# Performance work log

Measured on AMD Instinct MI355X. Metric: run time of the kernel, lower is better.

The kernel has to match this reference:

```python
import jax, jax.numpy as jnp
import numpy as np

EMBED_DIM = 64
NUM_GROUPS = 16
KEY_DIM = 64
WAVE_LENGTH = 1000.0


def setup_inputs() -> dict:
    key = jax.random.key(0)
    ks = jax.random.split(key, 8)
    N, R, D = 4, 512, 1024
    features = jax.random.normal(ks[0], (N, R, D), dtype=jnp.float32)
    # valid boxes: ymin/xmin in [0,800), heights/widths in [1,201)
    u = jax.random.uniform(ks[1], (N, R, 4), dtype=jnp.float32)
    ymin = u[..., 0] * 800.0
    xmin = u[..., 1] * 800.0
    ymax = ymin + 1.0 + u[..., 2] * 200.0
    xmax = xmin + 1.0 + u[..., 3] * 200.0
    boxes = jnp.stack([ymin, xmin, ymax, xmax], axis=-1)  # [N,R,4]
    s = 0.02
    geo_w = jax.random.normal(ks[2], (EMBED_DIM, NUM_GROUPS), dtype=jnp.float32) * s
    geo_b = jnp.zeros((NUM_GROUPS,), dtype=jnp.float32)
    Wq = jax.random.normal(ks[3], (D, KEY_DIM), dtype=jnp.float32) * s
    bq = jnp.zeros((KEY_DIM,), dtype=jnp.float32)
    Wk = jax.random.normal(ks[4], (D, KEY_DIM), dtype=jnp.float32) * s
    bk = jnp.zeros((KEY_DIM,), dtype=jnp.float32)
    Wv = jax.random.normal(ks[5], (D, D // NUM_GROUPS), dtype=jnp.float32) * s
    bv = jnp.zeros((D // NUM_GROUPS,), dtype=jnp.float32)
    return {"features": features, "boxes": boxes, "geo_w": geo_w, "geo_b": geo_b,
            "Wq": Wq, "bq": bq, "Wk": Wk, "bk": bk, "Wv": Wv, "bv": bv}


def _geometry_embeddings(boxes):
    # boxes: [N,R,4] -> embeddings [N,R,R,EMBED_DIM]
    ymin, xmin, ymax, xmax = jnp.split(boxes, 4, axis=2)  # each [N,R,1]
    height = ymax - ymin + 1.0
    width = xmax - xmin + 1.0
    cy = 0.5 * (ymin + ymax)
    cx = 0.5 * (xmin + xmax)
    cyT = jnp.transpose(cy, (0, 2, 1))
    cxT = jnp.transpose(cx, (0, 2, 1))
    dy = jnp.log(jnp.maximum((cy - cyT) / height, 1e-5))          # [N,R,R]
    dx = jnp.log(jnp.maximum((cx - cxT) / width, 1e-5))
    dh = jnp.log(height / jnp.transpose(height, (0, 2, 1)))
    dw = jnp.log(width / jnp.transpose(width, (0, 2, 1)))
    pos = jnp.stack([dy, dx, dh, dw], axis=3)                     # [N,R,R,4]
    feat_range = jnp.arange(EMBED_DIM // 8, dtype=jnp.float32)
    dim_mat = jnp.power(WAVE_LENGTH, (8.0 / EMBED_DIM) * feat_range)  # [8]
    div = (100.0 * pos)[..., None] / dim_mat                      # [N,R,R,4,8]
    emb = jnp.concatenate([jnp.sin(div), jnp.cos(div)], axis=4)   # [N,R,R,4,16]
    N, R = boxes.shape[0], boxes.shape[1]
    return emb.reshape(N, R, R, EMBED_DIM)


def reference(features, boxes, geo_w, geo_b, Wq, bq, Wk, bk, Wv, bv):
    N, R, D = features.shape
    G = NUM_GROUPS
    dk = KEY_DIM // G  # per-group key dim
    emb = _geometry_embeddings(boxes)                              # [N,R,R,E]
    # 1x1 conv + relu over pairwise embedding channels
    geometry_weight = jax.nn.relu(jnp.einsum('nqke,eg->nqkg', emb, geo_w) + geo_b)
    geometry_weight = jnp.transpose(geometry_weight, (0, 1, 3, 2))  # [N,R,G,R]
    q = (features @ Wq + bq).reshape(N, R, G, dk)
    k = (features @ Wk + bk).reshape(N, R, G, dk)
    v = features @ Wv + bv                                          # [N,R,D/G]
    dot = jnp.einsum('nqgd,nkgd->ngqk', q, k) / jnp.sqrt(jnp.float32(dk))
    appearance_weight = jnp.transpose(dot, (0, 2, 1, 3))            # [N,R,G,R]
    relation = jnp.log(jnp.maximum(geometry_weight, 1e-6)) + appearance_weight
    relation = jax.nn.softmax(relation, axis=3)                     # [N,R,G,R]
    out = jnp.einsum('nqgk,nkv->nqgv', relation, v)                 # [N,R,G,D/G]
    out = out.reshape(N, R, D)
    return features + out
```

## Files before the change

### kernel.cpp

```cpp
#include <hip/hip_runtime.h>
#include <stdint.h>

#define R_ 512
#define D_ 1024
#define G_ 16
#define NT 256

typedef __attribute__((ext_vector_type(8))) short short8;
typedef __attribute__((ext_vector_type(4))) float floatx4;

#if __has_builtin(__builtin_amdgcn_fractf)
#define FRACT(x) __builtin_amdgcn_fractf(x)
#else
#define FRACT(x) ((x) - floorf(x))
#endif

__device__ __forceinline__ unsigned pk2bf(float a, float b) {
    unsigned ua = __builtin_bit_cast(unsigned, a) + 0x8000u;
    unsigned ub = __builtin_bit_cast(unsigned, b) + 0x8000u;
    return (ub & 0xFFFF0000u) | (ua >> 16);
}
__device__ __forceinline__ unsigned short f2bf(float a) {
    return (unsigned short)((__builtin_bit_cast(unsigned, a) + 0x8000u) >> 16);
}

__global__ __launch_bounds__(256) void prep_kernel(
    const float* __restrict__ Wq, const float* __restrict__ Wk,
    const float* __restrict__ Wv, const float* __restrict__ geo_w,
    const float* __restrict__ boxes,
    unsigned short* __restrict__ WTb, unsigned short* __restrict__ geoF,
    float4* __restrict__ bp4, float2* __restrict__ bp2, int NR)
{
    const int b = blockIdx.x, t = threadIdx.x;
    if (b < 48) {
        __shared__ float s[64][65];
        const int mat = b >> 4, rblk = b & 15;
        const float* Wsrc = (mat == 0) ? Wq : (mat == 1) ? Wk : Wv;
        const int d0 = rblk * 64;
        #pragma unroll
        for (int i = 0; i < 16; i++) {
            int e = t + i * 256;
            s[e >> 6][e & 63] = Wsrc[(size_t)(d0 + (e >> 6)) * 64 + (e & 63)];
        }
        __syncthreads();
        #pragma unroll
        for (int i = 0; i < 16; i++) {
            int e = t + i * 256;
            int c = e >> 6, r = e & 63;
            WTb[(size_t)(mat * 64 + c) * 1024 + d0 + r] = f2bf(s[r][c]);
        }
    } else if (b == 48) {
        #pragma unroll
        for (int i = 0; i < 4; i++) {
            int idx = t * 4 + i;
            int h = idx >> 9, rem = idx & 511, ll = rem >> 3, j = rem & 7;
            int e = h * 32 + (ll >> 4) * 8 + j, cc = ll & 15;
            geoF[idx] = f2bf(geo_w[e * G_ + cc]);
        }
    } else {
        int r = (b - 49) * 256 + t;
        if (r < NR) {
            float ymin = boxes[r*4+0], xmin = boxes[r*4+1];
            float ymax = boxes[r*4+2], xmax = boxes[r*4+3];
            float h = ymax - ymin + 1.0f, w = xmax - xmin + 1.0f;
            bp4[r] = make_float4(0.5f * (ymin + ymax), 0.5f * (xmin + xmax),
                                 __logf(h), __logf(w));
            bp2[r] = make_float2(1.0f / h, 1.0f / w);
        }
    }
}

__global__ __launch_bounds__(256) void proj_kernel(
    const float* __restrict__ feat, const unsigned short* __restrict__ WTb,
    const float* __restrict__ bq, const float* __restrict__ bk,
    const float* __restrict__ bv,
    unsigned short* __restrict__ qd16, unsigned short* __restrict__ kb16,
    unsigned short* __restrict__ vT16)
{
    __shared__ __align__(16) unsigned short s_A[16][1032];

    const int t = threadIdx.x, l = t & 63, w = t >> 6;
    const int mb = blockIdx.x / 3, ng = blockIdx.x % 3;
    const long row0 = (long)mb * 16;

    const float4* f4 = (const float4*)(feat + row0 * D_);
    #pragma unroll
    for (int i = 0; i < 16; i++) {
        int e = t + i * 256;
        int row = e >> 8, c4 = e & 255;
        float4 v = f4[e];
        uint2 pk;
        pk.x = pk2bf(v.x, v.y);
        pk.y = pk2bf(v.z, v.w);
        *(uint2*)&s_A[row][c4 * 4] = pk;
    }
    __syncthreads();

    const int lc = l & 15, q = l >> 4;
    const int gcol = (ng * 4 + w) * 16 + lc;
    const unsigned short* bptr = WTb + (size_t)gcol * 1024 + q * 8;

    floatx4 acc = {0.f, 0.f, 0.f, 0.f};
    #pragma unroll 8
    for (int k0 = 0; k0 < 1024; k0 += 32) {
        short8 a  = *(const short8*)&s_A[lc][k0 + q * 8];
        short8 bb = *(const short8*)(bptr + k0);
        acc = __builtin_amdgcn_mfma_f32_16x16x32_bf16(a, bb, acc, 0, 0, 0);
    }

    const int mat = gcol >> 6, mcol = gcol & 63;
    const float* B = (mat == 0) ? bq : (mat == 1) ? bk : bv;
    const float bias = B[mcol];
    #pragma unroll
    for (int r = 0; r < 4; r++) {
        long gr = row0 + q * 4 + r;
        float val = acc[r] + bias;
        if (mat == 0)      qd16[gr * 64 + mcol] = f2bf(0.5f * val);
        else if (mat == 1) kb16[gr * 64 + mcol] = f2bf(val);
        else               vT16[((size_t)((gr >> 9) * 64 + mcol)) * 512 + (gr & 511)] = f2bf(val);
    }
}

__global__ __launch_bounds__(256, 4) void relation_kernel(
    const float* __restrict__ feat, const float* __restrict__ geo_b,
    const unsigned short* __restrict__ geoF, const unsigned short* __restrict__ qd16,
    const unsigned short* __restrict__ kb16, const unsigned short* __restrict__ vT16,
    const float4* __restrict__ bp4, const float2* __restrict__ bp2,
    float* __restrict__ out)
{
    __shared__ __align__(16) unsigned short s_p[2][16][520];
    __shared__ float s_reds[2][4][16];

    const int t = threadIdx.x;
    const int l = t & 63;
    const int w = t >> 6;
    const int c = l & 15;
    const int quad = l >> 4;
    const int nqA = blockIdx.x * 2, nqB = nqA + 1;
    const int n = nqA >> 9;

    const float4 qbA = bp4[nqA], qbB = bp4[nqB];
    const float2 qiA = bp2[nqA], qiB = bp2[nqB];
    const float gbias = geo_b[c];
    const floatx4 ginit = {gbias, gbias, gbias, gbias};

    short8 bgeo0 = *(const short8*)(geoF + l * 8);
    short8 bgeo1 = *(const short8*)(geoF + 512 + l * 8);

    const bool act = (quad == ((c >> 1) & 3));
    const int hsel = c >> 3, jhalf = c & 1;
    uint2 qvA = *(const uint2*)(qd16 + (size_t)nqA * 64 + c * 4);
    uint2 qvB = *(const uint2*)(qd16 + (size_t)nqB * 64 + c * 4);
    short qA[4] = {(short)(qvA.x & 0xFFFF), (short)(qvA.x >> 16),
                   (short)(qvA.y & 0xFFFF), (short)(qvA.y >> 16)};
    short qB[4] = {(short)(qvB.x & 0xFFFF), (short)(qvB.x >> 16),
                   (short)(qvB.y & 0xFFFF), (short)(qvB.y >> 16)};
    short8 bqfA0, bqfA1, bqfB0, bqfB1;
    #pragma unroll
    for (int j = 0; j < 8; j++) {
        bool on0 = act && (hsel == 0) && ((j >> 2) == jhalf);
        bool on1 = act && (hsel == 1) && ((j >> 2) == jhalf);
        bqfA0[j] = on0 ? qA[j & 3] : (short)0;
        bqfA1[j] = on1 ? qA[j & 3] : (short)0;
        bqfB0[j] = on0 ? qB[j & 3] : (short)0;
        bqfB1[j] = on1 ? qB[j & 3] : (short)0;
    }

    const float C8[8] = {
        15.91549431f,
        15.91549431f * 0.4216965034f,
        15.91549431f * 0.1778279410f,
        15.91549431f * 0.0749894209f,
        15.91549431f * 0.0316227766f,
        15.91549431f * 0.0133352143f,
        15.91549431f * 0.0056234133f,
        15.91549431f * 0.0023713737f };

    const float offs = (quad & 1) ? 0.25f : 0.0f;
    const bool qlow = (quad < 2);

    float sumA = 0.f, sumB = 0.f;
    const int krow0 = n * R_ + w * 128;

    #pragma unroll
    for (int ti = 0; ti < 8; ti++) {
        float4 kb = bp4[krow0 + ti * 16 + c];

        float aA  = qlow ? (qbA.x - kb.x) * qiA.x : (qbA.y - kb.y) * qiA.y;
        float pAa = __logf(fmaxf(aA, 1e-5f));
        float pAb = qlow ? (qbA.z - kb.z) : (qbA.w - kb.w);
        float aB  = qlow ? (qbB.x - kb.x) * qiB.x : (qbB.y - kb.y) * qiB.y;
        float pBa = __logf(fmaxf(aB, 1e-5f));
        float pBb = qlow ? (qbB.z - kb.z) : (qbB.w - kb.w);

        uint4 uA0, uA1, uB0, uB1;
        #pragma unroll
        for (int jj = 0; jj < 4; jj++) {
            float r0, r1;
            r0 = FRACT(fmaf(pAa, C8[2*jj],   offs));
            r1 = FRACT(fmaf(pAa, C8[2*jj+1], offs));
            (&uA0.x)[jj] = pk2bf(__builtin_amdgcn_sinf(r0), __builtin_amdgcn_sinf(r1));
            r0 = FRACT(fmaf(pAb, C8[2*jj],   offs));
            r1 = FRACT(fmaf(pAb, C8[2*jj+1], offs));
            (&uA1.x)[jj] = pk2bf(__builtin_amdgcn_sinf(r0), __builtin_amdgcn_sinf(r1));
            r0 = FRACT(fmaf(pBa, C8[2*jj],   offs));
            r1 = FRACT(fmaf(pBa, C8[2*jj+1], offs));
            (&uB0.x)[jj] = pk2bf(__builtin_amdgcn_sinf(r0), __builtin_amdgcn_sinf(r1));
            r0 = FRACT(fmaf(pBb, C8[2*jj],   offs));
            r1 = FRACT(fmaf(pBb, C8[2*jj+1], offs));
            (&uB1.x)[jj] = pk2bf(__builtin_amdgcn_sinf(r0), __builtin_amdgcn_sinf(r1));
        }
        short8 aeA0 = __builtin_bit_cast(short8, uA0);
        short8 aeA1 = __builtin_bit_cast(short8, uA1);
        short8 aeB0 = __builtin_bit_cast(short8, uB0);
        short8 aeB1 = __builtin_bit_cast(short8, uB1);

        const unsigned short* kr = kb16 + (size_t)(krow0 + ti * 16 + c) * 64;
        short8 ak0 = *(const short8*)(kr + quad * 8);
        short8 ak1 = *(const short8*)(kr + 32 + quad * 8);

        floatx4 accgA = ginit, acckA = {0,0,0,0};
        floatx4 accgB = ginit, acckB = {0,0,0,0};
        accgA = __builtin_amdgcn_mfma_f32_16x16x32_bf16(aeA0, bgeo0, accgA, 0, 0, 0);
        accgA = __builtin_amdgcn_mfma_f32_16x16x32_bf16(aeA1, bgeo1, accgA, 0, 0, 0);
        accgB = __builtin_amdgcn_mfma_f32_16x16x32_bf16(aeB0, bgeo0, accgB, 0, 0, 0);
        accgB = __builtin_amdgcn_mfma_f32_16x16x32_bf16(aeB1, bgeo1, accgB, 0, 0, 0);
        acckA = __builtin_amdgcn_mfma_f32_16x16x32_bf16(ak0, bqfA0, acckA, 0, 0, 0);
        acckA = __builtin_amdgcn_mfma_f32_16x16x32_bf16(ak1, bqfA1, acckA, 0, 0, 0);
        acckB = __builtin_amdgcn_mfma_f32_16x16x32_bf16(ak0, bqfB0, acckB, 0, 0, 0);
        acckB = __builtin_amdgcn_mfma_f32_16x16x32_bf16(ak1, bqfB1, acckB, 0, 0, 0);

        int k0 = w * 128 + ti * 16 + quad * 4;
        float eA0 = fmaxf(accgA[0], 1e-6f) * __expf(acckA[0]);
        float eA1 = fmaxf(accgA[1], 1e-6f) * __expf(acckA[1]);
        float eA2 = fmaxf(accgA[2], 1e-6f) * __expf(acckA[2]);
        float eA3 = fmaxf(accgA[3], 1e-6f) * __expf(acckA[3]);
        sumA += (eA0 + eA1) + (eA2 + eA3);
        uint2 pkA; pkA.x = pk2bf(eA0, eA1); pkA.y = pk2bf(eA2, eA3);
        *(uint2*)&s_p[0][c][k0] = pkA;

        float eB0 = fmaxf(accgB[0], 1e-6f) * __expf(acckB[0]);
        float eB1 = fmaxf(accgB[1], 1e-6f) * __expf(acckB[1]);
        float eB2 = fmaxf(accgB[2], 1e-6f) * __expf(acckB[2]);
        float eB3 = fmaxf(accgB[3], 1e-6f) * __expf(acckB[3]);
        sumB += (eB0 + eB1) + (eB2 + eB3);
        uint2 pkB; pkB.x = pk2bf(eB0, eB1); pkB.y = pk2bf(eB2, eB3);
        *(uint2*)&s_p[1][c][k0] = pkB;
    }

    sumA += __shfl_xor(sumA, 16);
    sumA += __shfl_xor(sumA, 32);
    sumB += __shfl_xor(sumB, 16);
    sumB += __shfl_xor(sumB, 32);
    if (l < 16) { s_reds[0][w][l] = sumA; s_reds[1][w][l] = sumB; }
    __syncthreads();

    floatx4 accpA = {0,0,0,0}, accpB = {0,0,0,0};
    const unsigned short* vrow = vT16 + ((size_t)(n * 64 + w * 16 + c)) * 512;
    #pragma unroll
    for (int ks = 0; ks < 16; ks++) {
        short8 bv8 = *(const short8*)(vrow + ks * 32 + quad * 8);
        short8 apA = *(const short8*)(&s_p[0][c][ks * 32 + quad * 8]);
        short8 apB = *(const short8*)(&s_p[1][c][ks * 32 + quad * 8]);
        accpA = __builtin_amdgcn_mfma_f32_16x16x32_bf16(apA, bv8, accpA, 0, 0, 0);
        accpB = __builtin_amdgcn_mfma_f32_16x16x32_bf16(apB, bv8, accpB, 0, 0, 0);
    }

    #pragma unroll
    for (int r = 0; r < 4; r++) {
        int gg = quad * 4 + r;
        float sA = (s_reds[0][0][gg] + s_reds[0][1][gg]) + (s_reds[0][2][gg] + s_reds[0][3][gg]);
        float sB = (s_reds[1][0][gg] + s_reds[1][1][gg]) + (s_reds[1][2][gg] + s_reds[1][3][gg]);
        size_t oA = (size_t)nqA * D_ + (size_t)gg * 64 + w * 16 + c;
        size_t oB = (size_t)nqB * D_ + (size_t)gg * 64 + w * 16 + c;
        out[oA] = feat[oA] + accpA[r] / sA;
        out[oB] = feat[oB] + accpB[r] / sB;
    }
}

extern "C" void kernel_launch(void* const* d_in, const int* in_sizes, int n_in,
                              void* d_out, int out_size, void* d_ws, size_t ws_size,
                              hipStream_t stream) {
    const float* feat  = (const float*)d_in[0];
    const float* boxes = (const float*)d_in[1];
    const float* geo_w = (const float*)d_in[2];
    const float* geo_b = (const float*)d_in[3];
    const float* Wq    = (const float*)d_in[4];
    const float* bq    = (const float*)d_in[5];
    const float* Wk    = (const float*)d_in[6];
    const float* bk    = (const float*)d_in[7];
    const float* Wv    = (const float*)d_in[8];
    const float* bv    = (const float*)d_in[9];
    float* out = (float*)d_out;

    const int N  = in_sizes[0] / (R_ * D_);
    const int NR = N * R_;

    float4* bp4 = (float4*)d_ws;
    float2* bp2 = (float2*)(bp4 + NR);
    unsigned short* kb16 = (unsigned short*)(bp2 + NR);
    unsigned short* vT16 = kb16 + (size_t)NR * 64;
    unsigned short* qd16 = vT16 + (size_t)NR * 64;
    unsigned short* WTb  = qd16 + (size_t)NR * 64;
    unsigned short* geoF = WTb + (size_t)192 * 1024;

    prep_kernel<<<dim3(49 + (NR + 255) / 256), dim3(NT), 0, stream>>>(
        Wq, Wk, Wv, geo_w, boxes, WTb, geoF, bp4, bp2, NR);
    proj_kernel<<<dim3((NR / 16) * 3), dim3(NT), 0, stream>>>(
        feat, WTb, bq, bk, bv, qd16, kb16, vT16);
    relation_kernel<<<dim3(NR / 2), dim3(NT), 0, stream>>>(
        feat, geo_b, geoF, qd16, kb16, vT16, bp4, bp2, out);
}
```

Measured before the change: 48.88 us.

## Split relation kernel's two query rows across separate wave groups in 512-thread blocks

New measurement: 64.54 us. 32.0% more time.

```diff
diff --git a/kernel.cpp b/kernel.cpp
--- a/kernel.cpp
+++ b/kernel.cpp
@@ -121,7 +121,7 @@
     }
 }
 
-__global__ __launch_bounds__(256, 4) void relation_kernel(
+__global__ __launch_bounds__(512, 5) void relation_kernel(
     const float* __restrict__ feat, const float* __restrict__ geo_b,
     const unsigned short* __restrict__ geoF, const unsigned short* __restrict__ qd16,
     const unsigned short* __restrict__ kb16, const unsigned short* __restrict__ vT16,
@@ -133,14 +133,16 @@
 
     const int t = threadIdx.x;
     const int l = t & 63;
-    const int w = t >> 6;
+    const int wid = t >> 6;
+    const int row = wid >> 2;
+    const int w = wid & 3;
     const int c = l & 15;
     const int quad = l >> 4;
-    const int nqA = blockIdx.x * 2, nqB = nqA + 1;
-    const int n = nqA >> 9;
-
-    const float4 qbA = bp4[nqA], qbB = bp4[nqB];
-    const float2 qiA = bp2[nqA], qiB = bp2[nqB];
+    const int nq = blockIdx.x * 2 + row;
+    const int n = nq >> 9;
+
+    const float4 qb = bp4[nq];
+    const float2 qi = bp2[nq];
     const float gbias = geo_b[c];
     const floatx4 ginit = {gbias, gbias, gbias, gbias};
 
@@ -149,21 +151,16 @@
 
     const bool act = (quad == ((c >> 1) & 3));
     const int hsel = c >> 3, jhalf = c & 1;
-    uint2 qvA = *(const uint2*)(qd16 + (size_t)nqA * 64 + c * 4);
-    uint2 qvB = *(const uint2*)(qd16 + (size_t)nqB * 64 + c * 4);
-    short qA[4] = {(short)(qvA.x & 0xFFFF), (short)(qvA.x >> 16),
-                   (short)(qvA.y & 0xFFFF), (short)(qvA.y >> 16)};
-    short qB[4] = {(short)(qvB.x & 0xFFFF), (short)(qvB.x >> 16),
-                   (short)(qvB.y & 0xFFFF), (short)(qvB.y >> 16)};
-    short8 bqfA0, bqfA1, bqfB0, bqfB1;
+    uint2 qv = *(const uint2*)(qd16 + (size_t)nq * 64 + c * 4);
+    short qr[4] = {(short)(qv.x & 0xFFFF), (short)(qv.x >> 16),
+                   (short)(qv.y & 0xFFFF), (short)(qv.y >> 16)};
+    short8 bqf0, bqf1;
     #pragma unroll
     for (int j = 0; j < 8; j++) {
         bool on0 = act && (hsel == 0) && ((j >> 2) == jhalf);
         bool on1 = act && (hsel == 1) && ((j >> 2) == jhalf);
-        bqfA0[j] = on0 ? qA[j & 3] : (short)0;
-        bqfA1[j] = on1 ? qA[j & 3] : (short)0;
-        bqfB0[j] = on0 ? qB[j & 3] : (short)0;
-        bqfB1[j] = on1 ? qB[j & 3] : (short)0;
+        bqf0[j] = on0 ? qr[j & 3] : (short)0;
+        bqf1[j] = on1 ? qr[j & 3] : (short)0;
     }
 
     const float C8[8] = {
@@ -179,102 +176,72 @@
     const float offs = (quad & 1) ? 0.25f : 0.0f;
     const bool qlow = (quad < 2);
 
-    float sumA = 0.f, sumB = 0.f;
+    float sum = 0.f;
     const int krow0 = n * R_ + w * 128;
 
     #pragma unroll
     for (int ti = 0; ti < 8; ti++) {
         float4 kb = bp4[krow0 + ti * 16 + c];
 
-        float aA  = qlow ? (qbA.x - kb.x) * qiA.x : (qbA.y - kb.y) * qiA.y;
-        float pAa = __logf(fmaxf(aA, 1e-5f));
-        float pAb = qlow ? (qbA.z - kb.z) : (qbA.w - kb.w);
-        float aB  = qlow ? (qbB.x - kb.x) * qiB.x : (qbB.y - kb.y) * qiB.y;
-        float pBa = __logf(fmaxf(aB, 1e-5f));
-        float pBb = qlow ? (qbB.z - kb.z) : (qbB.w - kb.w);
-
-        uint4 uA0, uA1, uB0, uB1;
+        float a    = qlow ? (qb.x - kb.x) * qi.x : (qb.y - kb.y) * qi.y;
+        float posa = __logf(fmaxf(a, 1e-5f));
+        float posb = qlow ? (qb.z - kb.z) : (qb.w - kb.w);
+
+        uint4 u0, u1;
         #pragma unroll
         for (int jj = 0; jj < 4; jj++) {
             float r0, r1;
-            r0 = FRACT(fmaf(pAa, C8[2*jj],   offs));
-            r1 = FRACT(fmaf(pAa, C8[2*jj+1], offs));
-            (&uA0.x)[jj] = pk2bf(__builtin_amdgcn_sinf(r0), __builtin_amdgcn_sinf(r1));
-            r0 = FRACT(fmaf(pAb, C8[2*jj],   offs));
-            r1 = FRACT(fmaf(pAb, C8[2*jj+1], offs));
-            (&uA1.x)[jj] = pk2bf(__builtin_amdgcn_sinf(r0), __builtin_amdgcn_sinf(r1));
-            r0 = FRACT(fmaf(pBa, C8[2*jj],   offs));
-            r1 = FRACT(fmaf(pBa, C8[2*jj+1], offs));
-            (&uB0.x)[jj] = pk2bf(__builtin_amdgcn_sinf(r0), __builtin_amdgcn_sinf(r1));
-            r0 = FRACT(fmaf(pBb, C8[2*jj],   offs));
-            r1 = FRACT(fmaf(pBb, C8[2*jj+1], offs));
-            (&uB1.x)[jj] = pk2bf(__builtin_amdgcn_sinf(r0), __builtin_amdgcn_sinf(r1));
-        }
-        short8 aeA0 = __builtin_bit_cast(short8, uA0);
-        short8 aeA1 = __builtin_bit_cast(short8, uA1);
-        short8 aeB0 = __builtin_bit_cast(short8, uB0);
-        short8 aeB1 = __builtin_bit_cast(short8, uB1);
+            r0 = FRACT(fmaf(posa, C8[2*jj],   offs));
+            r1 = FRACT(fmaf(posa, C8[2*jj+1], offs));
+            (&u0.x)[jj] = pk2bf(__builtin_amdgcn_sinf(r0), __builtin_amdgcn_sinf(r1));
+            r0 = FRACT(fmaf(posb, C8[2*jj],   offs));
+            r1 = FRACT(fmaf(posb, C8[2*jj+1], offs));
+            (&u1.x)[jj] = pk2bf(__builtin_amdgcn_sinf(r0), __builtin_amdgcn_sinf(r1));
+        }
+        short8 ae0 = __builtin_bit_cast(short8, u0);
+        short8 ae1 = __builtin_bit_cast(short8, u1);
 
         const unsigned short* kr = kb16 + (size_t)(krow0 + ti * 16 + c) * 64;
         short8 ak0 = *(const short8*)(kr + quad * 8);
         short8 ak1 = *(const short8*)(kr + 32 + quad * 8);
 
-        floatx4 accgA = ginit, acckA = {0,0,0,0};
-        floatx4 accgB = ginit, acckB = {0,0,0,0};
-        accgA = __builtin_amdgcn_mfma_f32_16x16x32_bf16(aeA0, bgeo0, accgA, 0, 0, 0);
-        accgA = __builtin_amdgcn_mfma_f32_16x16x32_bf16(aeA1, bgeo1, accgA, 0, 0, 0);
-        accgB = __builtin_amdgcn_mfma_f32_16x16x32_bf16(aeB0, bgeo0, accgB, 0, 0, 0);
-        accgB = __builtin_amdgcn_mfma_f32_16x16x32_bf16(aeB1, bgeo1, accgB, 0, 0, 0);
-        acckA = __builtin_amdgcn_mfma_f32_16x16x32_bf16(ak0, bqfA0, acckA, 0, 0, 0);
-        acckA = __builtin_amdgcn_mfma_f32_16x16x32_bf16(ak1, bqfA1, acckA, 0, 0, 0);
-        acckB = __builtin_amdgcn_mfma_f32_16x16x32_bf16(ak0, bqfB0, acckB, 0, 0, 0);
-        acckB = __builtin_amdgcn_mfma_f32_16x16x32_bf16(ak1, bqfB1, acckB, 0, 0, 0);
+        floatx4 accg = ginit, acck = {0,0,0,0};
+        accg = __builtin_amdgcn_mfma_f32_16x16x32_bf16(ae0, bgeo0, accg, 0, 0, 0);
+        accg = __builtin_amdgcn_mfma_f32_16x16x32_bf16(ae1, bgeo1, accg, 0, 0, 0);
+        acck = __builtin_amdgcn_mfma_f32_16x16x32_bf16(ak0, bqf0, acck, 0, 0, 0);
+        acck = __builtin_amdgcn_mfma_f32_16x16x32_bf16(ak1, bqf1, acck, 0, 0, 0);
 
         int k0 = w * 128 + ti * 16 + quad * 4;
-        float eA0 = fmaxf(accgA[0], 1e-6f) * __expf(acckA[0]);
-        float eA1 = fmaxf(accgA[1], 1e-6f) * __expf(acckA[1]);
-        float eA2 = fmaxf(accgA[2], 1e-6f) * __expf(acckA[2]);
-        float eA3 = fmaxf(accgA[3], 1e-6f) * __expf(acckA[3]);
-        sumA += (eA0 + eA1) + (eA2 + eA3);
-        uint2 pkA; pkA.x = pk2bf(eA0, eA1); pkA.y = pk2bf(eA2, eA3);
-        *(uint2*)&s_p[0][c][k0] = pkA;
-
-        float eB0 = fmaxf(accgB[0], 1e-6f) * __expf(acckB[0]);
-        float eB1 = fmaxf(accgB[1], 1e-6f) * __expf(acckB[1]);
-        float eB2 = fmaxf(accgB[2], 1e-6f) * __expf(acckB[2]);
-        float eB3 = fmaxf(accgB[3], 1e-6f) * __expf(acckB[3]);
-        sumB += (eB0 + eB1) + (eB2 + eB3);
-        uint2 pkB; pkB.x = pk2bf(eB0, eB1); pkB.y = pk2bf(eB2, eB3);
-        *(uint2*)&s_p[1][c][k0] = pkB;
-    }
-
-    sumA += __shfl_xor(sumA, 16);
-    sumA += __shfl_xor(sumA, 32);
-    sumB += __shfl_xor(sumB, 16);
-    sumB += __shfl_xor(sumB, 32);
-    if (l < 16) { s_reds[0][w][l] = sumA; s_reds[1][w][l] = sumB; }
+        float e0 = fmaxf(accg[0], 1e-6f) * __expf(acck[0]);
+        float e1 = fmaxf(accg[1], 1e-6f) * __expf(acck[1]);
+        float e2 = fmaxf(accg[2], 1e-6f) * __expf(acck[2]);
+        float e3 = fmaxf(accg[3], 1e-6f) * __expf(acck[3]);
+        sum += (e0 + e1) + (e2 + e3);
+        uint2 pk; pk.x = pk2bf(e0, e1); pk.y = pk2bf(e2, e3);
+        *(uint2*)&s_p[row][c][k0] = pk;
+    }
+
+    sum += __shfl_xor(sum, 16);
+    sum += __shfl_xor(sum, 32);
+    if (l < 16) s_reds[row][w][l] = sum;
     __syncthreads();
 
-    floatx4 accpA = {0,0,0,0}, accpB = {0,0,0,0};
+    floatx4 accp = {0,0,0,0};
     const unsigned short* vrow = vT16 + ((size_t)(n * 64 + w * 16 + c)) * 512;
     #pragma unroll
     for (int ks = 0; ks < 16; ks++) {
         short8 bv8 = *(const short8*)(vrow + ks * 32 + quad * 8);
-        short8 apA = *(const short8*)(&s_p[0][c][ks * 32 + quad * 8]);
-        short8 apB = *(const short8*)(&s_p[1][c][ks * 32 + quad * 8]);
-        accpA = __builtin_amdgcn_mfma_f32_16x16x32_bf16(apA, bv8, accpA, 0, 0, 0);
-        accpB = __builtin_amdgcn_mfma_f32_16x16x32_bf16(apB, bv8, accpB, 0, 0, 0);
+        short8 ap  = *(const short8*)(&s_p[row][c][ks * 32 + quad * 8]);
+        accp = __builtin_amdgcn_mfma_f32_16x16x32_bf16(ap, bv8, accp, 0, 0, 0);
     }
 
     #pragma unroll
     for (int r = 0; r < 4; r++) {
         int gg = quad * 4 + r;
-        float sA = (s_reds[0][0][gg] + s_reds[0][1][gg]) + (s_reds[0][2][gg] + s_reds[0][3][gg]);
-        float sB = (s_reds[1][0][gg] + s_reds[1][1][gg]) + (s_reds[1][2][gg] + s_reds[1][3][gg]);
-        size_t oA = (size_t)nqA * D_ + (size_t)gg * 64 + w * 16 + c;
-        size_t oB = (size_t)nqB * D_ + (size_t)gg * 64 + w * 16 + c;
-        out[oA] = feat[oA] + accpA[r] / sA;
-        out[oB] = feat[oB] + accpB[r] / sB;
+        float s = (s_reds[row][0][gg] + s_reds[row][1][gg])
+                + (s_reds[row][2][gg] + s_reds[row][3][gg]);
+        size_t o = (size_t)nq * D_ + (size_t)gg * 64 + w * 16 + c;
+        out[o] = feat[o] + accp[r] / s;
     }
 }
 
@@ -308,6 +275,6 @@
         Wq, Wk, Wv, geo_w, boxes, WTb, geoF, bp4, bp2, NR);
     proj_kernel<<<dim3((NR / 16) * 3), dim3(NT), 0, stream>>>(
         feat, WTb, bq, bk, bv, qd16, kb16, vT16);
-    relation_kernel<<<dim3(NR / 2), dim3(NT), 0, stream>>>(
+    relation_kernel<<<dim3(NR / 2), dim3(512), 0, stream>>>(
         feat, geo_b, geoF, qd16, kb16, vT16, bp4, bp2, out);
 }
```
